# Optimization experiments

Measured on AMD Instinct MI355X. Metric: run time of the kernel, lower is better.

Reference implementation:

```python
import jax, jax.numpy as jnp
import numpy as np

EMBED_DIM = 1024
NUM_HEADS = 16
HEAD_DIM = EMBED_DIM // NUM_HEADS


def setup_inputs() -> dict:
    key = jax.random.key(0)
    kx, kq, kk, kv, ko = jax.random.split(key, 5)
    scale = 1.0 / np.sqrt(EMBED_DIM)
    return {
        "x": jax.random.normal(kx, (4, 2048, EMBED_DIM), dtype=jnp.float32),
        # nn.Linear weights are [out, in]; y = x @ W.T
        "w_q": jax.random.normal(kq, (EMBED_DIM, EMBED_DIM), dtype=jnp.float32) * scale,
        "w_k": jax.random.normal(kk, (EMBED_DIM, EMBED_DIM), dtype=jnp.float32) * scale,
        "w_v": jax.random.normal(kv, (EMBED_DIM, EMBED_DIM), dtype=jnp.float32) * scale,
        "w_o": jax.random.normal(ko, (EMBED_DIM, EMBED_DIM), dtype=jnp.float32) * scale,
    }


def reference(x, w_q, w_k, w_v, w_o):
    b, s, _ = x.shape
    # projections (Linear with no bias: x @ W.T)
    q = (x @ w_q.T).reshape(b, s, NUM_HEADS, HEAD_DIM).transpose(0, 2, 1, 3)
    k = (x @ w_k.T).reshape(b, s, NUM_HEADS, HEAD_DIM).transpose(0, 2, 1, 3)
    v = (x @ w_v.T).reshape(b, s, NUM_HEADS, HEAD_DIM).transpose(0, 2, 1, 3)
    # scores: [b, h, s, s]
    scores = jnp.einsum("bhqd,bhkd->bhqk", q, k) / jnp.sqrt(jnp.float32(HEAD_DIM)).astype(x.dtype)
    attn = jax.nn.softmax(scores, axis=-1)
    out = jnp.einsum("bhqk,bhkd->bhqd", attn, v)  # [b, h, s, d]
    out = out.transpose(0, 2, 1, 3).reshape(b, s, EMBED_DIM)
    return out @ w_o.T
```

## Files before the change

kernel.cpp:

```cpp
#include <hip/hip_runtime.h>
#include <math.h>

#define EMBED 1024
#define NHEAD 16
#define HDIM  64
#define BATCH 4
#define SEQ   2048
#define MROWS (BATCH * SEQ)

typedef __attribute__((ext_vector_type(8))) short short8;
typedef __attribute__((ext_vector_type(4))) float floatx4;

#if __has_builtin(__builtin_amdgcn_exp2f)
#define EXP2(x) __builtin_amdgcn_exp2f(x)
#else
#define EXP2(x) exp2f(x)
#endif

__device__ __forceinline__ unsigned short f2bf(float f) {
  unsigned u = __float_as_uint(f);
  u += 0x7fffu + ((u >> 16) & 1u);
  return (unsigned short)(u >> 16);
}

__device__ __forceinline__ unsigned short f2bf_fast(float f) {
  return (unsigned short)((__float_as_uint(f) + 0x8000u) >> 16);
}

__device__ __forceinline__ void gl_lds16(const void* g, void* l) {
  __builtin_amdgcn_global_load_lds(
      (const __attribute__((address_space(1))) unsigned int*)g,
      (__attribute__((address_space(3))) unsigned int*)l, 16, 0, 0);
}

__global__ __launch_bounds__(256) void cast_bf16_kernel(
    const float* __restrict__ x,  const float* __restrict__ wq,
    const float* __restrict__ wk, const float* __restrict__ wv,
    const float* __restrict__ wo,
    unsigned short* __restrict__ xb, unsigned short* __restrict__ wb) {
  const size_t NX = (size_t)MROWS * EMBED;
  size_t i4 = ((size_t)blockIdx.x * 256 + threadIdx.x) * 4;
  const float* src;
  unsigned short* dst;
  size_t off;
  if (i4 < NX) {
    src = x; dst = xb; off = i4;
  } else {
    size_t j = i4 - NX;
    int r = (int)(j >> 20);
    off = j & ((1u << 20) - 1);
    src = (r == 0) ? wq : (r == 1) ? wk : (r == 2) ? wv : wo;
    dst = wb + ((size_t)r << 20);
  }
  float4 v = *(const float4*)(src + off);
  ushort4 o;
  o.x = f2bf(v.x); o.y = f2bf(v.y); o.z = f2bf(v.z); o.w = f2bf(v.w);
  *(ushort4*)(dst + off) = o;
}

__device__ __forceinline__ void gemm_core(
    const unsigned short* __restrict__ Amat,
    const unsigned short* __restrict__ Bmat,
    int mBase, int nBase,
    unsigned short* As, unsigned short* Bs,
    floatx4 acc[4][4]) {
  const int t = threadIdx.x;
  const int lane = t & 63, w = t >> 6;
  const int wr = w >> 1, wc = w & 1;
  const int quad = lane >> 4, l15 = lane & 15;

  const int f0 = (w * 2 + 0) * 64 + lane;
  const int f1 = (w * 2 + 1) * 64 + lane;
  const unsigned short* ga0 = Amat + (size_t)(mBase + (f0 >> 2)) * EMBED + (f0 & 3) * 8;
  const unsigned short* ga1 = Amat + (size_t)(mBase + (f1 >> 2)) * EMBED + (f1 & 3) * 8;
  const unsigned short* gb0 = Bmat + (size_t)(nBase + (f0 >> 2)) * EMBED + (f0 & 3) * 8;
  const unsigned short* gb1 = Bmat + (size_t)(nBase + (f1 >> 2)) * EMBED + (f1 & 3) * 8;
  unsigned short* la0 = As + (w * 2 + 0) * 512;
  unsigned short* la1 = As + (w * 2 + 1) * 512;
  unsigned short* lb0 = Bs + (w * 2 + 0) * 512;
  unsigned short* lb1 = Bs + (w * 2 + 1) * 512;

  for (int kb = 0; kb < EMBED; kb += 32) {
    __syncthreads();
    gl_lds16(ga0 + kb, la0);
    gl_lds16(ga1 + kb, la1);
    gl_lds16(gb0 + kb, lb0);
    gl_lds16(gb1 + kb, lb1);
    __syncthreads();
    short8 a[4], b[4];
#pragma unroll
    for (int mi = 0; mi < 4; ++mi)
      a[mi] = *(const short8*)&As[(wr * 64 + mi * 16 + l15) * 32 + quad * 8];
#pragma unroll
    for (int ni = 0; ni < 4; ++ni)
      b[ni] = *(const short8*)&Bs[(wc * 64 + ni * 16 + l15) * 32 + quad * 8];
#pragma unroll
    for (int mi = 0; mi < 4; ++mi)
#pragma unroll
      for (int ni = 0; ni < 4; ++ni)
        acc[mi][ni] = __builtin_amdgcn_mfma_f32_16x16x32_bf16(
            a[mi], b[ni], acc[mi][ni], 0, 0, 0);
  }
}

__global__ __launch_bounds__(256) void proj_qkv_bf16(
    const unsigned short* __restrict__ xb,
    const unsigned short* __restrict__ wb,
    unsigned short* __restrict__ qkv) {
  const int which = blockIdx.z;
  const unsigned short* W = wb + ((size_t)which << 20);
  const int nBase = blockIdx.x * 128;
  const int mBase = blockIdx.y * 128;

  __shared__ unsigned short As[128 * 32];
  __shared__ unsigned short Bs[128 * 32];

  floatx4 acc[4][4] = {};
  gemm_core(xb, W, mBase, nBase, As, Bs, acc);

  const int t = threadIdx.x;
  const int lane = t & 63, w = t >> 6;
  const int wr = w >> 1, wc = w & 1;
  const int quad = lane >> 4, l15 = lane & 15;

  unsigned short* out = qkv + (size_t)which * MROWS * EMBED;
  if (which < 2) {
    const float scale = (which == 0) ? 0.18033688f : 1.0f;
#pragma unroll
    for (int mi = 0; mi < 4; ++mi)
#pragma unroll
      for (int ni = 0; ni < 4; ++ni) {
        const int n = nBase + wc * 64 + ni * 16 + l15;
        const int h = n >> 6, d = n & 63;
#pragma unroll
        for (int r = 0; r < 4; ++r) {
          const int m = mBase + wr * 64 + mi * 16 + quad * 4 + r;
          const int b = m >> 11, s = m & (SEQ - 1);
          out[(((size_t)(b * NHEAD + h) * SEQ) + s) * HDIM + d] =
              f2bf(acc[mi][ni][r] * scale);
        }
      }
  } else {
#pragma unroll
    for (int mi = 0; mi < 4; ++mi) {
      const int m0 = mBase + wr * 64 + mi * 16 + quad * 4;
      const int b = m0 >> 11, s0 = m0 & (SEQ - 1);
#pragma unroll
      for (int ni = 0; ni < 4; ++ni) {
        const int n = nBase + wc * 64 + ni * 16 + l15;
        const int h = n >> 6, d = n & 63;
        ushort4 pk;
        pk.x = f2bf(acc[mi][ni][0]); pk.y = f2bf(acc[mi][ni][1]);
        pk.z = f2bf(acc[mi][ni][2]); pk.w = f2bf(acc[mi][ni][3]);
        *(ushort4*)&out[((size_t)(b * NHEAD + h) * HDIM + d) * SEQ + s0] = pk;
      }
    }
  }
}

__global__ __launch_bounds__(256) void attn_mfma(
    const unsigned short* __restrict__ qkv,
    unsigned short* __restrict__ aout) {
  const unsigned short* Q = qkv;
  const unsigned short* K = qkv + (size_t)MROWS * EMBED;
  const unsigned short* V = qkv + 2 * (size_t)MROWS * EMBED;

  const int bh = blockIdx.y;
  const int qBase = blockIdx.x * 64;

  __shared__ unsigned short Ks[64 * 64];
  __shared__ unsigned short Vs[64 * 64];
  __shared__ unsigned short Ps[64 * 72];

  const int t = threadIdx.x;
  const int lane = t & 63, w = t >> 6;
  const int quad = lane >> 4, l15 = lane & 15;

  const unsigned short* qrow = Q + ((size_t)bh * SEQ + qBase + w * 16 + l15) * HDIM;
  short8 qa0 = *(const short8*)(qrow + quad * 8);
  short8 qa1 = *(const short8*)(qrow + 32 + quad * 8);

  const int f0 = (w * 2 + 0) * 64 + lane;
  const int f1 = (w * 2 + 1) * 64 + lane;
  const int kr0 = f0 >> 3, kg0 = (f0 & 7) ^ (kr0 & 7);
  const int kr1 = f1 >> 3, kg1 = (f1 & 7) ^ (kr1 & 7);
  const unsigned short* kbase = K + (size_t)bh * SEQ * HDIM;
  const unsigned short* vbase = V + (size_t)bh * HDIM * SEQ;
  const unsigned short* gk0 = kbase + (size_t)kr0 * HDIM + kg0 * 8;
  const unsigned short* gk1 = kbase + (size_t)kr1 * HDIM + kg1 * 8;
  const unsigned short* gv0 = vbase + (size_t)kr0 * SEQ + kg0 * 8;
  const unsigned short* gv1 = vbase + (size_t)kr1 * SEQ + kg1 * 8;
  unsigned short* lk0 = Ks + (w * 2 + 0) * 512;
  unsigned short* lk1 = Ks + (w * 2 + 1) * 512;
  unsigned short* lv0 = Vs + (w * 2 + 0) * 512;
  unsigned short* lv1 = Vs + (w * 2 + 1) * 512;

  floatx4 o[4] = {};
  floatx4 osum = {0.f, 0.f, 0.f, 0.f};

  const short one_bf = (short)0x3F80;
  const short8 ones = {one_bf, one_bf, one_bf, one_bf,
                       one_bf, one_bf, one_bf, one_bf};

  for (int kt = 0; kt < SEQ; kt += 64) {
    __syncthreads();
    gl_lds16(gk0 + (size_t)kt * HDIM, lk0);
    gl_lds16(gk1 + (size_t)kt * HDIM, lk1);
    gl_lds16(gv0 + kt, lv0);
    gl_lds16(gv1 + kt, lv1);
    __syncthreads();

    floatx4 s[4] = {};
#pragma unroll
    for (int ni = 0; ni < 4; ++ni) {
      const int key = ni * 16 + l15;
      short8 b0 = *(const short8*)&Ks[key * 64 + ((quad) ^ (key & 7)) * 8];
      s[ni] = __builtin_amdgcn_mfma_f32_16x16x32_bf16(qa0, b0, s[ni], 0, 0, 0);
      short8 b1 = *(const short8*)&Ks[key * 64 + ((4 + quad) ^ (key & 7)) * 8];
      s[ni] = __builtin_amdgcn_mfma_f32_16x16x32_bf16(qa1, b1, s[ni], 0, 0, 0);
    }

#pragma unroll
    for (int ni = 0; ni < 4; ++ni)
#pragma unroll
      for (int r = 0; r < 4; ++r)
        Ps[(w * 16 + quad * 4 + r) * 72 + ni * 16 + l15] =
            f2bf_fast(EXP2(s[ni][r]));

    short8 pa0 = *(const short8*)&Ps[(w * 16 + l15) * 72 + quad * 8];
    short8 pa1 = *(const short8*)&Ps[(w * 16 + l15) * 72 + 32 + quad * 8];
#pragma unroll
    for (int nv = 0; nv < 4; ++nv) {
      const int vd = nv * 16 + l15;
      short8 b0 = *(const short8*)&Vs[vd * 64 + ((quad) ^ (vd & 7)) * 8];
      o[nv] = __builtin_amdgcn_mfma_f32_16x16x32_bf16(pa0, b0, o[nv], 0, 0, 0);
      short8 b1 = *(const short8*)&Vs[vd * 64 + ((4 + quad) ^ (vd & 7)) * 8];
      o[nv] = __builtin_amdgcn_mfma_f32_16x16x32_bf16(pa1, b1, o[nv], 0, 0, 0);
    }
    osum = __builtin_amdgcn_mfma_f32_16x16x32_bf16(pa0, ones, osum, 0, 0, 0);
    osum = __builtin_amdgcn_mfma_f32_16x16x32_bf16(pa1, ones, osum, 0, 0, 0);
  }

  float inv[4];
#pragma unroll
  for (int r = 0; r < 4; ++r) inv[r] = 1.0f / osum[r];

  const int b = bh >> 4, h = bh & 15;
#pragma unroll
  for (int nv = 0; nv < 4; ++nv)
#pragma unroll
    for (int r = 0; r < 4; ++r)
      aout[((size_t)b * SEQ + qBase + w * 16 + quad * 4 + r) * EMBED +
           h * HDIM + nv * 16 + l15] = f2bf(o[nv][r] * inv[r]);
}

__global__ __launch_bounds__(256) void out_proj_bf16(
    const unsigned short* __restrict__ aout,
    const unsigned short* __restrict__ wb,
    float* __restrict__ Cout) {
  const int nBase = blockIdx.x * 128;
  const int mBase = blockIdx.y * 128;

  __shared__ unsigned short As[128 * 32];
  __shared__ unsigned short Bs[128 * 32];

  floatx4 acc[4][4] = {};
  gemm_core(aout, wb + ((size_t)3 << 20), mBase, nBase, As, Bs, acc);

  const int t = threadIdx.x;
  const int lane = t & 63, w = t >> 6;
  const int wr = w >> 1, wc = w & 1;
  const int quad = lane >> 4, l15 = lane & 15;

#pragma unroll
  for (int mi = 0; mi < 4; ++mi)
#pragma unroll
    for (int ni = 0; ni < 4; ++ni) {
      const int n = nBase + wc * 64 + ni * 16 + l15;
#pragma unroll
      for (int r = 0; r < 4; ++r) {
        const int m = mBase + wr * 64 + mi * 16 + quad * 4 + r;
        Cout[(size_t)m * EMBED + n] = acc[mi][ni][r];
      }
    }
}

extern "C" void kernel_launch(void* const* d_in, const int* in_sizes, int n_in,
                              void* d_out, int out_size, void* d_ws, size_t ws_size,
                              hipStream_t stream) {
  const float* x  = (const float*)d_in[0];
  const float* wq = (const float*)d_in[1];
  const float* wk = (const float*)d_in[2];
  const float* wv = (const float*)d_in[3];
  const float* wo = (const float*)d_in[4];
  float* out = (float*)d_out;

  char* ws = (char*)d_ws;
  unsigned short* xb   = (unsigned short*)(ws);
  unsigned short* wb   = (unsigned short*)(ws + (16u << 20));
  unsigned short* qkv  = (unsigned short*)(ws + (26u << 20));
  unsigned short* aout = (unsigned short*)(ws + (76u << 20));

  cast_bf16_kernel<<<12288, 256, 0, stream>>>(x, wq, wk, wv, wo, xb, wb);
  proj_qkv_bf16<<<dim3(EMBED / 128, MROWS / 128, 3), 256, 0, stream>>>(xb, wb, qkv);
  attn_mfma<<<dim3(SEQ / 64, BATCH * NHEAD), 256, 0, stream>>>(qkv, aout);
  out_proj_bf16<<<dim3(EMBED / 128, MROWS / 128), 256, 0, stream>>>(aout, wb, out);
}
```

Before: 319.6 us.

## Rework attention with 32x32 MFMA, transposed scores, register-resident P

```diff
diff --git a/kernel.cpp b/kernel.cpp
--- a/kernel.cpp
+++ b/kernel.cpp
@@ -10,6 +10,7 @@
 
 typedef __attribute__((ext_vector_type(8))) short short8;
 typedef __attribute__((ext_vector_type(4))) float floatx4;
+typedef __attribute__((ext_vector_type(16))) float floatx16;
 
 #if __has_builtin(__builtin_amdgcn_exp2f)
 #define EXP2(x) __builtin_amdgcn_exp2f(x)
@@ -23,8 +24,9 @@
   return (unsigned short)(u >> 16);
 }
 
-__device__ __forceinline__ unsigned short f2bf_fast(float f) {
-  return (unsigned short)((__float_as_uint(f) + 0x8000u) >> 16);
+__device__ __forceinline__ unsigned pack2bf(float lo, float hi) {
+  return ((__float_as_uint(lo) + 0x8000u) >> 16) |
+         ((__float_as_uint(hi) + 0x8000u) & 0xffff0000u);
 }
 
 __device__ __forceinline__ void gl_lds16(const void* g, void* l) {
@@ -166,19 +168,22 @@
   const unsigned short* V = qkv + 2 * (size_t)MROWS * EMBED;
 
   const int bh = blockIdx.y;
-  const int qBase = blockIdx.x * 64;
+  const int qBase = blockIdx.x * 128;
 
   __shared__ unsigned short Ks[64 * 64];
   __shared__ unsigned short Vs[64 * 64];
-  __shared__ unsigned short Ps[64 * 72];
 
   const int t = threadIdx.x;
   const int lane = t & 63, w = t >> 6;
-  const int quad = lane >> 4, l15 = lane & 15;
-
-  const unsigned short* qrow = Q + ((size_t)bh * SEQ + qBase + w * 16 + l15) * HDIM;
-  short8 qa0 = *(const short8*)(qrow + quad * 8);
-  short8 qa1 = *(const short8*)(qrow + 32 + quad * 8);
+  const int h2 = lane >> 5;
+  const int q31 = lane & 31;
+
+  const unsigned short* qrow =
+      Q + ((size_t)bh * SEQ + qBase + w * 32 + q31) * HDIM;
+  short8 qa[4];
+#pragma unroll
+  for (int ds = 0; ds < 4; ++ds)
+    qa[ds] = *(const short8*)(qrow + ds * 16 + h2 * 8);
 
   const int f0 = (w * 2 + 0) * 64 + lane;
   const int f1 = (w * 2 + 1) * 64 + lane;
@@ -195,12 +200,12 @@
   unsigned short* lv0 = Vs + (w * 2 + 0) * 512;
   unsigned short* lv1 = Vs + (w * 2 + 1) * 512;
 
-  floatx4 o[4] = {};
-  floatx4 osum = {0.f, 0.f, 0.f, 0.f};
+  floatx16 ot0 = {}, ot1 = {};
+  floatx16 osum = {};
 
   const short one_bf = (short)0x3F80;
-  const short8 ones = {one_bf, one_bf, one_bf, one_bf,
-                       one_bf, one_bf, one_bf, one_bf};
+  const short8 onesA = {one_bf, one_bf, one_bf, one_bf,
+                        one_bf, one_bf, one_bf, one_bf};
 
   for (int kt = 0; kt < SEQ; kt += 64) {
     __syncthreads();
@@ -210,48 +215,64 @@
     gl_lds16(gv1 + kt, lv1);
     __syncthreads();
 
-    floatx4 s[4] = {};
-#pragma unroll
-    for (int ni = 0; ni < 4; ++ni) {
-      const int key = ni * 16 + l15;
-      short8 b0 = *(const short8*)&Ks[key * 64 + ((quad) ^ (key & 7)) * 8];
-      s[ni] = __builtin_amdgcn_mfma_f32_16x16x32_bf16(qa0, b0, s[ni], 0, 0, 0);
-      short8 b1 = *(const short8*)&Ks[key * 64 + ((4 + quad) ^ (key & 7)) * 8];
-      s[ni] = __builtin_amdgcn_mfma_f32_16x16x32_bf16(qa1, b1, s[ni], 0, 0, 0);
-    }
-
-#pragma unroll
-    for (int ni = 0; ni < 4; ++ni)
-#pragma unroll
-      for (int r = 0; r < 4; ++r)
-        Ps[(w * 16 + quad * 4 + r) * 72 + ni * 16 + l15] =
-            f2bf_fast(EXP2(s[ni][r]));
-
-    short8 pa0 = *(const short8*)&Ps[(w * 16 + l15) * 72 + quad * 8];
-    short8 pa1 = *(const short8*)&Ps[(w * 16 + l15) * 72 + 32 + quad * 8];
-#pragma unroll
-    for (int nv = 0; nv < 4; ++nv) {
-      const int vd = nv * 16 + l15;
-      short8 b0 = *(const short8*)&Vs[vd * 64 + ((quad) ^ (vd & 7)) * 8];
-      o[nv] = __builtin_amdgcn_mfma_f32_16x16x32_bf16(pa0, b0, o[nv], 0, 0, 0);
-      short8 b1 = *(const short8*)&Vs[vd * 64 + ((4 + quad) ^ (vd & 7)) * 8];
-      o[nv] = __builtin_amdgcn_mfma_f32_16x16x32_bf16(pa1, b1, o[nv], 0, 0, 0);
-    }
-    osum = __builtin_amdgcn_mfma_f32_16x16x32_bf16(pa0, ones, osum, 0, 0, 0);
-    osum = __builtin_amdgcn_mfma_f32_16x16x32_bf16(pa1, ones, osum, 0, 0, 0);
-  }
-
-  float inv[4];
-#pragma unroll
-  for (int r = 0; r < 4; ++r) inv[r] = 1.0f / osum[r];
-
-  const int b = bh >> 4, h = bh & 15;
-#pragma unroll
-  for (int nv = 0; nv < 4; ++nv)
-#pragma unroll
-    for (int r = 0; r < 4; ++r)
-      aout[((size_t)b * SEQ + qBase + w * 16 + quad * 4 + r) * EMBED +
-           h * HDIM + nv * 16 + l15] = f2bf(o[nv][r] * inv[r]);
+    floatx16 st0 = {}, st1 = {};
+#pragma unroll
+    for (int ds = 0; ds < 4; ++ds) {
+      const int g = ds * 2 + h2;
+      short8 ka0 = *(const short8*)&Ks[q31 * 64 + ((g ^ (q31 & 7)) * 8)];
+      st0 = __builtin_amdgcn_mfma_f32_32x32x16_bf16(ka0, qa[ds], st0, 0, 0, 0);
+      const int k1 = 32 + q31;
+      short8 ka1 = *(const short8*)&Ks[k1 * 64 + ((g ^ (k1 & 7)) * 8)];
+      st1 = __builtin_amdgcn_mfma_f32_32x32x16_bf16(ka1, qa[ds], st1, 0, 0, 0);
+    }
+
+    unsigned pk0[8], pk1[8], sw0[8], sw1[8];
+#pragma unroll
+    for (int i = 0; i < 8; ++i) {
+      pk0[i] = pack2bf(EXP2(st0[2 * i]), EXP2(st0[2 * i + 1]));
+      sw0[i] = __shfl_xor(pk0[i], 32);
+      pk1[i] = pack2bf(EXP2(st1[2 * i]), EXP2(st1[2 * i + 1]));
+      sw1[i] = __shfl_xor(pk1[i], 32);
+    }
+
+#pragma unroll
+    for (int kst = 0; kst < 4; ++kst) {
+      const unsigned* pk = (kst < 2) ? pk0 : pk1;
+      const unsigned* sw = (kst < 2) ? sw0 : sw1;
+      const int kl = kst & 1;
+      union { unsigned u[4]; short8 s; } pb;
+      pb.u[0] = h2 ? sw[4 * kl + 2] : pk[4 * kl + 0];
+      pb.u[1] = h2 ? sw[4 * kl + 3] : pk[4 * kl + 1];
+      pb.u[2] = h2 ? pk[4 * kl + 2] : sw[4 * kl + 0];
+      pb.u[3] = h2 ? pk[4 * kl + 3] : sw[4 * kl + 1];
+
+      osum = __builtin_amdgcn_mfma_f32_32x32x16_bf16(onesA, pb.s, osum, 0, 0, 0);
+
+      const int g = kst * 2 + h2;
+      short8 va0 = *(const short8*)&Vs[q31 * 64 + ((g ^ (q31 & 7)) * 8)];
+      ot0 = __builtin_amdgcn_mfma_f32_32x32x16_bf16(va0, pb.s, ot0, 0, 0, 0);
+      const int d1 = 32 + q31;
+      short8 va1 = *(const short8*)&Vs[d1 * 64 + ((g ^ (d1 & 7)) * 8)];
+      ot1 = __builtin_amdgcn_mfma_f32_32x32x16_bf16(va1, pb.s, ot1, 0, 0, 0);
+    }
+  }
+
+  const float inv = 1.0f / osum[0];
+
+  const int b = bh >> 4, hh = bh & 15;
+  unsigned short* orow =
+      aout + ((size_t)b * SEQ + qBase + w * 32 + q31) * EMBED + hh * HDIM;
+#pragma unroll
+  for (int rg = 0; rg < 4; ++rg) {
+    const int d0 = rg * 8 + h2 * 4;
+    ushort4 p0, p1;
+    p0.x = f2bf(ot0[4 * rg + 0] * inv); p0.y = f2bf(ot0[4 * rg + 1] * inv);
+    p0.z = f2bf(ot0[4 * rg + 2] * inv); p0.w = f2bf(ot0[4 * rg + 3] * inv);
+    *(ushort4*)(orow + d0) = p0;
+    p1.x = f2bf(ot1[4 * rg + 0] * inv); p1.y = f2bf(ot1[4 * rg + 1] * inv);
+    p1.z = f2bf(ot1[4 * rg + 2] * inv); p1.w = f2bf(ot1[4 * rg + 3] * inv);
+    *(ushort4*)(orow + 32 + d0) = p1;
+  }
 }
 
 __global__ __launch_bounds__(256) void out_proj_bf16(
@@ -303,6 +324,6 @@
 
   cast_bf16_kernel<<<12288, 256, 0, stream>>>(x, wq, wk, wv, wo, xb, wb);
   proj_qkv_bf16<<<dim3(EMBED / 128, MROWS / 128, 3), 256, 0, stream>>>(xb, wb, qkv);
-  attn_mfma<<<dim3(SEQ / 64, BATCH * NHEAD), 256, 0, stream>>>(qkv, aout);
+  attn_mfma<<<dim3(SEQ / 128, BATCH * NHEAD), 256, 0, stream>>>(qkv, aout);
   out_proj_bf16<<<dim3(EMBED / 128, MROWS / 128), 256, 0, stream>>>(aout, wb, out);
 }
```

Measured after the change: 306.2 us. 4.2% less time.
